# Performance work log

Measured on AMD Instinct MI355X. Metric: run time of the kernel, lower is better.

Reference implementation:

```python
import jax, jax.numpy as jnp
import numpy as np

TEMPERATURE = 0.5
EPS = 1e-8  # matches F.cosine_similarity eps clamp


def setup_inputs() -> dict:
    key = jax.random.key(0)
    k1, k2 = jax.random.split(key)
    logits = jax.random.normal(k1, (8192, 256), dtype=jnp.float32)
    label = jax.random.randint(k2, (8192,), 0, 10, dtype=jnp.int64)
    return {"logits": logits, "label": label}


def reference(logits, label):
    n = label.shape[0]
    # pairwise cosine similarity via normalize + GEMM (same math as the
    # broadcasted F.cosine_similarity, without the O(n^2 d) intermediate)
    norms = jnp.maximum(jnp.linalg.norm(logits, axis=1, keepdims=True), EPS)
    xn = logits / norms                       # [n, d]
    sim_matrix = xn @ xn.T                    # [n, n]

    eye = jnp.eye(n, dtype=sim_matrix.dtype)
    mask = (label[:, None] == label[None, :]).astype(sim_matrix.dtype)  # same-label (incl. diag)

    e = jnp.exp(sim_matrix / TEMPERATURE) * (1.0 - eye)  # zero diagonal
    sim = mask * e                            # same-label positives
    no_sim_sum = jnp.sum(e - sim, axis=1)     # [n] row sums of different-label terms
    sim_sum = sim + no_sim_sum[:, None]       # denominator per entry
    ratio = sim / sim_sum

    # zeros (different-label entries) get +1 via (1 - mask), diagonal gets +1 via eye -> -log(1) = 0
    loss_mat = -jnp.log((1.0 - mask) + ratio + eye)
    return jnp.sum(loss_mat) / (2 * n)
```

## Files before the change

### kernel.cpp

```cpp
#include <hip/hip_runtime.h>
#include <cstdint>
#include <cstddef>

typedef __bf16 bf16x8 __attribute__((ext_vector_type(8)));
typedef float  f32x4  __attribute__((ext_vector_type(4)));

#define N_ROWS 8192
#define KDIM   256
#define TEMP_INV 2.0f
#define LOG2E  1.4426950408889634f
#define EXPC   (TEMP_INV * LOG2E)

__device__ __forceinline__ ushort f2bf(float x) {
    uint32_t u = __float_as_uint(x);
    u += 0x7fffu + ((u >> 16) & 1u);
    return (ushort)(u >> 16);
}

__global__ void build_perm(const int* __restrict__ label, int* __restrict__ perm,
                           int* __restrict__ labelPerm, int* __restrict__ classStart,
                           int* __restrict__ cumTiles)
{
    __shared__ int lcnt[256][10];
    __shared__ int cstart[11];
    __shared__ int ccount[10];
    const int tid = threadIdx.x;
    const int wave = tid >> 6, lane = tid & 63;
    const int beg = tid * 32, end = beg + 32;

    int loc[10] = {0,0,0,0,0,0,0,0,0,0};
    for (int i = beg; i < end; ++i) {
        int c = label[i]; c = (c < 0) ? 0 : (c > 9 ? 9 : c);
        loc[c]++;
    }
    #pragma unroll
    for (int c = 0; c < 10; ++c) lcnt[tid][c] = loc[c];
    __syncthreads();

    for (int c = wave; c < 10; c += 4) {
        int s0 = lcnt[lane*4+0][c], s1 = lcnt[lane*4+1][c];
        int s2 = lcnt[lane*4+2][c], s3 = lcnt[lane*4+3][c];
        int tot = s0 + s1 + s2 + s3;
        int incl = tot;
        #pragma unroll
        for (int d = 1; d < 64; d <<= 1) {
            int up = __shfl_up(incl, d, 64);
            if (lane >= d) incl += up;
        }
        int excl = incl - tot;
        lcnt[lane*4+0][c] = excl;
        lcnt[lane*4+1][c] = excl + s0;
        lcnt[lane*4+2][c] = excl + s0 + s1;
        lcnt[lane*4+3][c] = excl + s0 + s1 + s2;
        if (lane == 63) ccount[c] = incl;
    }
    __syncthreads();

    if (tid == 0) {
        int run = 0, runT = 0;
        for (int c = 0; c < 10; ++c) {
            cstart[c] = run; classStart[c] = run;
            int tpc = (ccount[c] + 127) >> 7;
            cumTiles[c] = runT;
            run  += ccount[c];
            runT += tpc * tpc;
        }
        cstart[10] = run; classStart[10] = run; cumTiles[10] = runT;
    }
    __syncthreads();

    int ofs[10];
    #pragma unroll
    for (int c = 0; c < 10; ++c) ofs[c] = lcnt[tid][c];
    for (int i = beg; i < end; ++i) {
        int c = label[i]; c = (c < 0) ? 0 : (c > 9 ? 9 : c);
        int pos = cstart[c] + ofs[c]++;
        perm[pos] = i;
        labelPerm[pos] = c;
    }
}

__global__ __launch_bounds__(256) void normalize_rows(const float* __restrict__ logits,
        const int* __restrict__ perm, ushort* __restrict__ xn)
{
    const int p = blockIdx.x * 4 + (threadIdx.x >> 6);
    const int lane = threadIdx.x & 63;
    const int old = perm[p];
    float4 v = reinterpret_cast<const float4*>(logits + (size_t)old * KDIM)[lane];
    float ss = v.x*v.x + v.y*v.y + v.z*v.z + v.w*v.w;
    #pragma unroll
    for (int off = 32; off >= 1; off >>= 1) ss += __shfl_xor(ss, off, 64);
    float inv = 1.0f / fmaxf(sqrtf(ss), 1e-8f);
    ushort4 o;
    o.x = f2bf(v.x * inv); o.y = f2bf(v.y * inv);
    o.z = f2bf(v.z * inv); o.w = f2bf(v.w * inv);
    reinterpret_cast<ushort4*>(xn + (size_t)p * KDIM)[lane] = o;
}

__device__ __forceinline__ void stage_tiles(const ushort* __restrict__ xn,
        int rowBase, int colBase, int kb, ushort* As, ushort* Bs, int wave, int lane)
{
    #pragma unroll
    for (int it = 0; it < 4; ++it) {
        int ci = it * 256 + wave * 64 + lane;
        int row = ci >> 3;
        int c = (ci & 7) ^ (row & 7);
        int rowA = rowBase + row; if (rowA > N_ROWS - 1) rowA = N_ROWS - 1;
        int rowB = colBase + row; if (rowB > N_ROWS - 1) rowB = N_ROWS - 1;
        const ushort* gA = xn + (size_t)rowA * KDIM + kb + c * 8;
        const ushort* gB = xn + (size_t)rowB * KDIM + kb + c * 8;
        ushort* lA = As + (size_t)(it * 256 + wave * 64) * 8;
        ushort* lB = Bs + (size_t)(it * 256 + wave * 64) * 8;
        __builtin_amdgcn_global_load_lds((const __attribute__((address_space(1))) void*)gA,
                                         (__attribute__((address_space(3))) void*)lA, 16, 0, 0);
        __builtin_amdgcn_global_load_lds((const __attribute__((address_space(1))) void*)gB,
                                         (__attribute__((address_space(3))) void*)lB, 16, 0, 0);
    }
}

__device__ __forceinline__ void compute_step(const ushort* As, const ushort* Bs,
        f32x4 acc[4][4], int wave, int lane)
{
    const int wr = wave >> 1, wc = wave & 1;
    const int lrow = lane & 15;
    const int kgrp = lane >> 4;
    #pragma unroll
    for (int kk = 0; kk < 2; ++kk) {
        bf16x8 a[4], b[4];
        const int c = kk * 4 + kgrp;
        #pragma unroll
        for (int mi = 0; mi < 4; ++mi) {
            const int row = wr*64 + mi*16 + lrow;
            a[mi] = *reinterpret_cast<const bf16x8*>(As + (size_t)row * 64 + ((c ^ (row & 7)) * 8));
        }
        #pragma unroll
        for (int ni = 0; ni < 4; ++ni) {
            const int row = wc*64 + ni*16 + lrow;
            b[ni] = *reinterpret_cast<const bf16x8*>(Bs + (size_t)row * 64 + ((c ^ (row & 7)) * 8));
        }
        #pragma unroll
        for (int mi = 0; mi < 4; ++mi)
            #pragma unroll
            for (int ni = 0; ni < 4; ++ni)
                acc[mi][ni] = __builtin_amdgcn_mfma_f32_16x16x32_bf16(a[mi], b[ni], acc[mi][ni], 0, 0, 0);
    }
}

#define K_LOOP(xn, rowBase, colBase, acc, wave, lane)                              \
    stage_tiles(xn, rowBase, colBase, 0, As0, Bs0, wave, lane);                    \
    __syncthreads();                                                               \
    _Pragma("unroll")                                                              \
    for (int kt = 0; kt < 4; ++kt) {                                               \
        ushort* Ac = (kt & 1) ? As1 : As0;                                         \
        ushort* Bc = (kt & 1) ? Bs1 : Bs0;                                         \
        if (kt < 3) stage_tiles(xn, rowBase, colBase, (kt + 1) * 64,               \
                                (kt & 1) ? As0 : As1, (kt & 1) ? Bs0 : Bs1,        \
                                wave, lane);                                       \
        compute_step(Ac, Bc, acc, wave, lane);                                     \
        if (kt < 3) __syncthreads();                                               \
    }

__global__ __launch_bounds__(256) void phase1_gemm(const ushort* __restrict__ xn,
        const int* __restrict__ labelPerm, float* __restrict__ pD)
{
    __shared__ __align__(16) char pool[65536];
    ushort* As0 = (ushort*)(pool);
    ushort* Bs0 = (ushort*)(pool + 16384);
    ushort* As1 = (ushort*)(pool + 32768);
    ushort* Bs1 = (ushort*)(pool + 49152);
    float* rowD = (float*)(pool);
    float* colD = (float*)(pool + 16384);
    __shared__ int rowLab[128], colLab[128];

    const int tid = threadIdx.x;
    const int wave = tid >> 6, lane = tid & 63;

    int t = blockIdx.x, bi = 0;
    while (t >= 64 - bi) { t -= 64 - bi; ++bi; }
    const int bj = bi + t;
    const bool isDiag = (bi == bj);
    const int rowBase = bi * 128, colBase = bj * 128;

    if (tid < 128) rowLab[tid] = labelPerm[rowBase + tid];
    else           colLab[tid - 128] = labelPerm[colBase + (tid - 128)];

    f32x4 acc[4][4] = {};
    K_LOOP(xn, rowBase, colBase, acc, wave, lane);

    const int wr = wave >> 1, wc = wave & 1;
    const int lrow = lane & 15, lgrp = lane >> 4;
    float colAcc[4] = {0.f, 0.f, 0.f, 0.f};
    #pragma unroll
    for (int mi = 0; mi < 4; ++mi) {
        #pragma unroll
        for (int reg = 0; reg < 4; ++reg) {
            const int tr = wr * 64 + mi * 16 + lgrp * 4 + reg;
            const int rl = rowLab[tr];
            float rowAcc = 0.f;
            #pragma unroll
            for (int ni = 0; ni < 4; ++ni) {
                const int tc = wc * 64 + ni * 16 + lrow;
                float e = __builtin_amdgcn_exp2f(acc[mi][ni][reg] * EXPC);
                float ed = (rl != colLab[tc]) ? e : 0.f;
                rowAcc += ed;
                colAcc[ni] += ed;
            }
            rowD[tr * 32 + wc * 16 + lrow] = rowAcc;
        }
    }
    if (!isDiag) {
        #pragma unroll
        for (int ni = 0; ni < 4; ++ni) {
            const int tc = wc * 64 + ni * 16 + lrow;
            colD[tc * 8 + wr * 4 + lgrp] = colAcc[ni];
        }
    }
    __syncthreads();

    if (tid < 128) {
        const float* p = rowD + tid * 32;
        float s = 0.f;
        #pragma unroll
        for (int k = 0; k < 8; ++k) {
            f32x4 v = *reinterpret_cast<const f32x4*>(p + k * 4);
            s += v[0] + v[1] + v[2] + v[3];
        }
        pD[(size_t)bj * N_ROWS + rowBase + tid] = s;
    } else if (!isDiag) {
        const int c2 = tid - 128;
        const float* p = colD + c2 * 8;
        f32x4 v0 = *reinterpret_cast<const f32x4*>(p);
        f32x4 v1 = *reinterpret_cast<const f32x4*>(p + 4);
        pD[(size_t)bi * N_ROWS + colBase + c2] =
            v0[0] + v0[1] + v0[2] + v0[3] + v1[0] + v1[1] + v1[2] + v1[3];
    }
}

__global__ void phase2_rowsum(const float* __restrict__ pD, float* __restrict__ Darr)
{
    const int i = blockIdx.x * blockDim.x + threadIdx.x;
    if (i >= N_ROWS) return;
    float d = 0.f;
    for (int tj = 0; tj < 64; ++tj) d += pD[(size_t)tj * N_ROWS + i];
    Darr[i] = d;
}

__global__ __launch_bounds__(256) void phase3_loss(const ushort* __restrict__ xn,
        const float* __restrict__ Darr, const int* __restrict__ classStart,
        const int* __restrict__ cumTiles, float* __restrict__ partial)
{
    __shared__ __align__(16) char pool[65536];
    ushort* As0 = (ushort*)(pool);
    ushort* Bs0 = (ushort*)(pool + 16384);
    ushort* As1 = (ushort*)(pool + 32768);
    ushort* Bs1 = (ushort*)(pool + 49152);
    __shared__ float red[256];

    const int b = blockIdx.x;
    const int nTiles = cumTiles[10];
    if (b >= nTiles) return;

    int c = 0;
    while (c < 9 && b >= cumTiles[c + 1]) ++c;
    const int s = classStart[c], e = classStart[c + 1];
    const int nc = e - s;
    const int tps = (nc + 127) >> 7;
    const int lt = b - cumTiles[c];
    const int ti = lt / tps, tj = lt - ti * tps;
    const int rowBase = s + ti * 128, colBase = s + tj * 128;

    const int tid = threadIdx.x;
    const int wave = tid >> 6, lane = tid & 63;

    f32x4 acc[4][4] = {};
    K_LOOP(xn, rowBase, colBase, acc, wave, lane);

    const int wr = wave >> 1, wc = wave & 1;
    const int lrow = lane & 15, lgrp = lane >> 4;
    float lsum = 0.f;
    #pragma unroll
    for (int mi = 0; mi < 4; ++mi) {
        #pragma unroll
        for (int reg = 0; reg < 4; ++reg) {
            const int r = rowBase + wr * 64 + mi * 16 + lgrp * 4 + reg;
            if (r < e) {
                const float Dr = Darr[r];
                #pragma unroll
                for (int ni = 0; ni < 4; ++ni) {
                    const int cg = colBase + wc * 64 + ni * 16 + lrow;
                    if (cg < e && cg != r) {
                        float sim = acc[mi][ni][reg];
                        float ev = __builtin_amdgcn_exp2f(sim * EXPC);
                        lsum += __logf(ev + Dr) - TEMP_INV * sim;
                    }
                }
            }
        }
    }
    red[tid] = lsum;
    __syncthreads();
    for (int st = 128; st > 0; st >>= 1) {
        if (tid < st) red[tid] += red[tid + st];
        __syncthreads();
    }
    if (tid == 0) partial[b] = red[0];
}

__global__ void phase4_final(const float* __restrict__ partial, const int* __restrict__ cumTiles,
                             float* __restrict__ out)
{
    __shared__ float red[256];
    const int tid = threadIdx.x;
    const int nTiles = cumTiles[10];
    float s = 0.f;
    for (int i = tid; i < nTiles; i += 256) s += partial[i];
    red[tid] = s;
    __syncthreads();
    for (int st = 128; st > 0; st >>= 1) {
        if (tid < st) red[tid] += red[tid + st];
        __syncthreads();
    }
    if (tid == 0) out[0] = red[0] * (1.0f / 16384.0f);
}

extern "C" void kernel_launch(void* const* d_in, const int* in_sizes, int n_in,
                              void* d_out, int out_size, void* d_ws, size_t ws_size,
                              hipStream_t stream)
{
    const float* logits = (const float*)d_in[0];
    const int*   label  = (const int*)d_in[1];
    float* out = (float*)d_out;

    char* ws = (char*)d_ws;
    ushort* xn        = (ushort*)(ws);
    float*  pD        = (float*)(ws + (4u << 20));
    float*  Darr      = (float*)(ws + (6u << 20));
    int*    perm      = (int*)(ws + (6u << 20) + (64u << 10));
    int*    labelPerm = (int*)(ws + (6u << 20) + (128u << 10));
    int*    classStart= (int*)(ws + (6u << 20) + (192u << 10));
    int*    cumTiles  = (int*)(ws + (6u << 20) + (192u << 10) + 256);
    float*  partial   = (float*)(ws + (6u << 20) + (256u << 10));

    hipLaunchKernelGGL(build_perm, dim3(1), dim3(256), 0, stream,
                       label, perm, labelPerm, classStart, cumTiles);
    hipLaunchKernelGGL(normalize_rows, dim3(2048), dim3(256), 0, stream,
                       logits, perm, xn);
    hipLaunchKernelGGL(phase1_gemm, dim3(2080), dim3(256), 0, stream,
                       xn, labelPerm, pD);
    hipLaunchKernelGGL(phase2_rowsum, dim3(32), dim3(256), 0, stream,
                       pD, Darr);
    hipLaunchKernelGGL(phase3_loss, dim3(4096), dim3(256), 0, stream,
                       xn, Darr, classStart, cumTiles, partial);
    hipLaunchKernelGGL(phase4_final, dim3(1), dim3(256), 0, stream,
                       partial, cumTiles, out);
}
```

Baseline: 75.26 us.

## Restructure GEMM K-loop into explicit two-deep pipeline with manual waitcnt and barriers

Replaces the double-buffered K loop with a hand-scheduled pipeline. Two tiles are prefetched up front, all LDS fragments are read into registers before the barrier so the buffer can be refilled, and MFMAs run at raised wave priority while the next global-to-LDS loads are in flight. It uses explicit vmcnt/lgkmcnt waits and sched barriers in place of __syncthreads. The label staging is merged into a single LDS array filled by one load per thread. The manual vmcnt counts rely on the exact number of loads per stage, so the scheme is fragile, and the label LDS write lacks an explicit sync before its later reads, which leans on the later barriers.

```diff
diff --git a/kernel.cpp b/kernel.cpp
--- a/kernel.cpp
+++ b/kernel.cpp
@@ -118,47 +118,86 @@
     }
 }
 
-__device__ __forceinline__ void compute_step(const ushort* As, const ushort* Bs,
-        f32x4 acc[4][4], int wave, int lane)
+__device__ __forceinline__ void read_frags(const ushort* As, const ushort* Bs,
+        bf16x8 (&a)[2][4], bf16x8 (&b)[2][4], int wave, int lane)
 {
     const int wr = wave >> 1, wc = wave & 1;
-    const int lrow = lane & 15;
-    const int kgrp = lane >> 4;
+    const int lrow = lane & 15, kgrp = lane >> 4;
     #pragma unroll
     for (int kk = 0; kk < 2; ++kk) {
-        bf16x8 a[4], b[4];
         const int c = kk * 4 + kgrp;
         #pragma unroll
         for (int mi = 0; mi < 4; ++mi) {
             const int row = wr*64 + mi*16 + lrow;
-            a[mi] = *reinterpret_cast<const bf16x8*>(As + (size_t)row * 64 + ((c ^ (row & 7)) * 8));
+            a[kk][mi] = *reinterpret_cast<const bf16x8*>(As + (size_t)row * 64 + ((c ^ (row & 7)) * 8));
         }
         #pragma unroll
         for (int ni = 0; ni < 4; ++ni) {
             const int row = wc*64 + ni*16 + lrow;
-            b[ni] = *reinterpret_cast<const bf16x8*>(Bs + (size_t)row * 64 + ((c ^ (row & 7)) * 8));
-        }
+            b[kk][ni] = *reinterpret_cast<const bf16x8*>(Bs + (size_t)row * 64 + ((c ^ (row & 7)) * 8));
+        }
+    }
+}
+
+__device__ __forceinline__ void mfma_frags(bf16x8 (&a)[2][4], bf16x8 (&b)[2][4],
+                                           f32x4 (&acc)[4][4])
+{
+    #pragma unroll
+    for (int kk = 0; kk < 2; ++kk)
         #pragma unroll
         for (int mi = 0; mi < 4; ++mi)
             #pragma unroll
             for (int ni = 0; ni < 4; ++ni)
-                acc[mi][ni] = __builtin_amdgcn_mfma_f32_16x16x32_bf16(a[mi], b[ni], acc[mi][ni], 0, 0, 0);
-    }
-}
-
-#define K_LOOP(xn, rowBase, colBase, acc, wave, lane)                              \
-    stage_tiles(xn, rowBase, colBase, 0, As0, Bs0, wave, lane);                    \
-    __syncthreads();                                                               \
-    _Pragma("unroll")                                                              \
-    for (int kt = 0; kt < 4; ++kt) {                                               \
-        ushort* Ac = (kt & 1) ? As1 : As0;                                         \
-        ushort* Bc = (kt & 1) ? Bs1 : Bs0;                                         \
-        if (kt < 3) stage_tiles(xn, rowBase, colBase, (kt + 1) * 64,               \
-                                (kt & 1) ? As0 : As1, (kt & 1) ? Bs0 : Bs1,        \
-                                wave, lane);                                       \
-        compute_step(Ac, Bc, acc, wave, lane);                                     \
-        if (kt < 3) __syncthreads();                                               \
-    }
+                acc[mi][ni] = __builtin_amdgcn_mfma_f32_16x16x32_bf16(a[kk][mi], b[kk][ni], acc[mi][ni], 0, 0, 0);
+}
+
+#define PIPE_READS_RELEASE(Ac, Bc)                                   \
+    bf16x8 a[2][4], b[2][4];                                         \
+    read_frags(Ac, Bc, a, b, wave, lane);                            \
+    __builtin_amdgcn_sched_barrier(0);                               \
+    asm volatile("s_waitcnt lgkmcnt(0)" ::: "memory");               \
+    __builtin_amdgcn_s_barrier();
+
+#define PIPE_MFMA()                                                  \
+    __builtin_amdgcn_s_setprio(1);                                   \
+    mfma_frags(a, b, acc);                                           \
+    __builtin_amdgcn_s_setprio(0);
+
+#define PIPE_TAIL(N)                                                 \
+    __builtin_amdgcn_sched_barrier(0);                               \
+    asm volatile("s_waitcnt vmcnt(" #N ")" ::: "memory");            \
+    __builtin_amdgcn_s_barrier();
+
+__device__ __forceinline__ void kloop_pipe(const ushort* __restrict__ xn,
+        int rowBase, int colBase, f32x4 (&acc)[4][4],
+        ushort* As0, ushort* Bs0, ushort* As1, ushort* Bs1, int wave, int lane)
+{
+    stage_tiles(xn, rowBase, colBase, 0,  As0, Bs0, wave, lane);
+    stage_tiles(xn, rowBase, colBase, 64, As1, Bs1, wave, lane);
+    asm volatile("s_waitcnt vmcnt(8)" ::: "memory");
+    __builtin_amdgcn_s_barrier();
+    {
+        PIPE_READS_RELEASE(As0, Bs0)
+        stage_tiles(xn, rowBase, colBase, 128, As0, Bs0, wave, lane);
+        PIPE_MFMA()
+        PIPE_TAIL(8)
+    }
+    {
+        PIPE_READS_RELEASE(As1, Bs1)
+        stage_tiles(xn, rowBase, colBase, 192, As1, Bs1, wave, lane);
+        PIPE_MFMA()
+        PIPE_TAIL(8)
+    }
+    {
+        PIPE_READS_RELEASE(As0, Bs0)
+        PIPE_MFMA()
+        PIPE_TAIL(0)
+    }
+    {
+        PIPE_READS_RELEASE(As1, Bs1)
+        PIPE_MFMA()
+    }
+}
 
 __global__ __launch_bounds__(256) void phase1_gemm(const ushort* __restrict__ xn,
         const int* __restrict__ labelPerm, float* __restrict__ pD)
@@ -170,7 +209,7 @@
     ushort* Bs1 = (ushort*)(pool + 49152);
     float* rowD = (float*)(pool);
     float* colD = (float*)(pool + 16384);
-    __shared__ int rowLab[128], colLab[128];
+    __shared__ int labLDS[256];
 
     const int tid = threadIdx.x;
     const int wave = tid >> 6, lane = tid & 63;
@@ -181,11 +220,11 @@
     const bool isDiag = (bi == bj);
     const int rowBase = bi * 128, colBase = bj * 128;
 
-    if (tid < 128) rowLab[tid] = labelPerm[rowBase + tid];
-    else           colLab[tid - 128] = labelPerm[colBase + (tid - 128)];
+    labLDS[tid] = labelPerm[(tid < 128) ? (rowBase + tid) : (colBase + tid - 128)];
+    __builtin_amdgcn_sched_barrier(0);
 
     f32x4 acc[4][4] = {};
-    K_LOOP(xn, rowBase, colBase, acc, wave, lane);
+    kloop_pipe(xn, rowBase, colBase, acc, As0, Bs0, As1, Bs1, wave, lane);
 
     const int wr = wave >> 1, wc = wave & 1;
     const int lrow = lane & 15, lgrp = lane >> 4;
@@ -195,13 +234,13 @@
         #pragma unroll
         for (int reg = 0; reg < 4; ++reg) {
             const int tr = wr * 64 + mi * 16 + lgrp * 4 + reg;
-            const int rl = rowLab[tr];
+            const int rl = labLDS[tr];
             float rowAcc = 0.f;
             #pragma unroll
             for (int ni = 0; ni < 4; ++ni) {
                 const int tc = wc * 64 + ni * 16 + lrow;
                 float e = __builtin_amdgcn_exp2f(acc[mi][ni][reg] * EXPC);
-                float ed = (rl != colLab[tc]) ? e : 0.f;
+                float ed = (rl != labLDS[128 + tc]) ? e : 0.f;
                 rowAcc += ed;
                 colAcc[ni] += ed;
             }
@@ -273,7 +312,7 @@
     const int wave = tid >> 6, lane = tid & 63;
 
     f32x4 acc[4][4] = {};
-    K_LOOP(xn, rowBase, colBase, acc, wave, lane);
+    kloop_pipe(xn, rowBase, colBase, acc, As0, Bs0, As1, Bs1, wave, lane);
 
     const int wr = wave >> 1, wc = wave & 1;
     const int lrow = lane & 15, lgrp = lane >> 4;
```

New measurement: 75.63 us. No clear change (+0.5%).
